# Optimization experiments

Measured on AMD Instinct MI355X. Metric: run time of the kernel, lower is better.

## Reference

```python
import jax, jax.numpy as jnp
import numpy as np

CDIM = 32
SCALES = (1, 16, 64, 256, 1024, 4096)  # last entry == T
INV_TEMP = 100.0
ENT_W = 0.1
COMMIT_W = 0.2
Q_SCALE = 1.0 / float(np.sqrt(CDIM))


def _interp_area(x, pt):
    # x: [B, T, C] -> [B, pt, C]; T divisible by pt so 'area' == block mean
    B, T, C = x.shape
    return x.reshape(B, pt, T // pt, C).mean(axis=2)


def _interp_linear(x, T):
    # x: [B, pt, C] -> [B, T, C]; mode='linear', align_corners=False
    pt = x.shape[1]
    pos = (jnp.arange(T, dtype=jnp.float32) + 0.5) * (pt / T) - 0.5
    pos = jnp.clip(pos, 0.0, pt - 1.0)
    lo = jnp.floor(pos).astype(jnp.int32)
    hi = jnp.minimum(lo + 1, pt - 1)
    w = (pos - lo.astype(jnp.float32))[None, :, None]
    return x[:, lo] * (1.0 - w) + x[:, hi] * w


def _bsq(f):
    # L2 normalize (torch F.normalize: clamp_min on norm)
    f = f / jnp.maximum(jnp.linalg.norm(f, axis=-1, keepdims=True), 1e-12)
    # sign quantize with STE
    zhat = jnp.where(f > 0, Q_SCALE, -Q_SCALE).astype(f.dtype)
    quantized = f + jax.lax.stop_gradient(zhat - f)
    # soft entropy loss
    p = jax.nn.sigmoid(-4.0 * f * (INV_TEMP / float(np.sqrt(CDIM))))
    prob = jnp.stack([p, 1.0 - p], axis=-1)  # [B, T, C, 2]
    ent = lambda c: -(c * jnp.log(c + 1e-8)).sum(axis=-1)
    per_sample_entropy = ent(prob).sum(axis=-1).mean()
    avg_prob = prob.mean(axis=(0, 1))  # [C, 2]
    cb_entropy = ent(avg_prob).sum()
    entropy_penalty = (per_sample_entropy - cb_entropy) / INV_TEMP
    commit = ((jax.lax.stop_gradient(quantized) - f) ** 2).sum(axis=-1).mean()
    aux = entropy_penalty * ENT_W + commit * COMMIT_W
    bits = (quantized > 0).astype(jnp.int32)
    return quantized, bits, aux


def setup_inputs() -> dict:
    key = jax.random.key(0)
    B, T, C = 128, SCALES[-1], CDIM
    return {"f_BTC": jax.random.normal(key, (B, T, C), dtype=jnp.float32)}


def reference(f_BTC):
    B, T, C = f_BTC.shape
    quantized_out = jnp.zeros_like(f_BTC)
    residual = f_BTC
    losses, bit_list = [], []
    for pt in SCALES:
        interp_res = _interp_area(residual, pt) if pt != T else residual
        q, bits, loss = _bsq(interp_res)
        q = _interp_linear(q, T) if pt != T else q
        residual = residual - jax.lax.stop_gradient(q)
        quantized_out = quantized_out + q
        bit_list.append(bits)
        losses.append(loss)
    all_losses = jnp.stack(losses, axis=-1)       # [num_scales]
    all_bits = jnp.concatenate(bit_list, axis=1)  # [B, sum(SCALES), C]
    return quantized_out, all_bits, all_losses
```

## Files before the change

### kernel.cpp

```cpp
#include <hip/hip_runtime.h>
#include <hip/hip_bf16.h>
#include <cstddef>
#include <cstdint>

#define NB 128
#define NT 4096
#define NC 32
#define BITROWS 5457
#define QV_ROWS 1361
#define QOUT_ELEMS (NB*NT*NC)
#define BITS_ELEMS (NB*BITROWS*NC)

#define ACC_OFF  22298624
#define S16_OFF  22302720

__device__ __constant__ float kQSC = 0.17677669529663687f;
__device__ __constant__ float kSIG = 17.67766952966369f;

__device__ __forceinline__ float interp_eval(const float* __restrict__ q, int P, int t, int c) {
  float pos = ((float)t + 0.5f) * ((float)P * (1.0f / 4096.0f)) - 0.5f;
  pos = fminf(fmaxf(pos, 0.0f), (float)(P - 1));
  const int lo = (int)pos;
  const int hi = min(lo + 1, P - 1);
  const float w = pos - (float)lo;
  const float a = __fmul_rn(q[lo * NC + c], 1.0f - w);
  const float b = __fmul_rn(q[hi * NC + c], w);
  return __fadd_rn(a, b);
}

__device__ __forceinline__ float interp_slice(const float* __restrict__ q, int P, int base, int t, int c) {
  float pos = ((float)t + 0.5f) * ((float)P * (1.0f / 4096.0f)) - 0.5f;
  pos = fminf(fmaxf(pos, 0.0f), (float)(P - 1));
  const int lo = (int)pos;
  const int hi = min(lo + 1, P - 1);
  const float w = pos - (float)lo;
  const float a = __fmul_rn(q[(lo - base) * NC + c], 1.0f - w);
  const float b = __fmul_rn(q[(hi - base) * NC + c], w);
  return __fadd_rn(a, b);
}

__device__ __forceinline__ void process_elem(
    float msum, float invn, int b, int rowOff, int j, int c,
    float* qlsRow, float* __restrict__ qvG, float* __restrict__ bitsG,
    float& entA, float& comA, float& pA)
{
  const float m = msum * invn;
  float ss = m * m;
  #pragma unroll
  for (int mk = 16; mk; mk >>= 1) ss += __shfl_xor(ss, mk, 32);
  const float den = fmaxf(sqrtf(ss), 1e-12f);
  const float fn = m / den;
  const bool bit = fn > 0.0f;
  const float zh = bit ? kQSC : -kQSC;
  const float qvv = fn + (zh - fn);
  if (qlsRow) qlsRow[c] = qvv;
  if (qvG) qvG[(size_t)b * (QV_ROWS * NC) + (size_t)(rowOff + j) * NC + c] = qvv;
  bitsG[(size_t)b * (BITROWS * NC) + (size_t)(rowOff + j) * NC + c] = bit ? 1.0f : 0.0f;
  const float arg = (-4.0f * fn) * kSIG;
  const float p = 1.0f / (1.0f + __expf(-arg));
  const float ent = -(p * __logf(p + 1e-8f) + (1.0f - p) * __logf((1.0f - p) + 1e-8f));
  const float d = qvv - fn;
  entA += ent; comA += d * d; pA += p;
}

__device__ __forceinline__ void reduce_losses(
    int sIdx, float entA, float comA, float pA, int tid, int nWaves,
    double* __restrict__ acc, float* redE, float* redC, float* redP)
{
  float e = entA, cm = comA;
  #pragma unroll
  for (int mk = 32; mk; mk >>= 1) { e += __shfl_xor(e, mk, 64); cm += __shfl_xor(cm, mk, 64); }
  const float p = pA + __shfl_xor(pA, 32, 64);
  const int w = tid >> 6, lane = tid & 63;
  if (lane == 0) { redE[w] = e; redC[w] = cm; }
  if (lane < 32) redP[w * 32 + lane] = p;
  __syncthreads();
  if (tid == 0) {
    double te = 0.0, tc = 0.0;
    for (int i = 0; i < nWaves; ++i) { te += (double)redE[i]; tc += (double)redC[i]; }
    atomicAdd(&acc[sIdx], te);
    atomicAdd(&acc[6 + sIdx], tc);
  }
  if (tid < 32) {
    float tp = 0.0f;
    for (int i = 0; i < nWaves; ++i) tp += redP[i * 32 + tid];
    atomicAdd(&acc[12 + sIdx * 32 + tid], (double)tp);
  }
  __syncthreads();
}

__global__ __launch_bounds__(256) void k_sum16(const float* __restrict__ f, float* __restrict__ S16) {
  const int idx = blockIdx.x * 256 + threadIdx.x;
  if (idx >= NB * 256 * NC) return;
  const int c = idx & 31;
  const int j = (idx >> 5) & 255;
  const int b = idx >> 13;
  const float* p = f + (size_t)b * (NT * NC) + (size_t)j * 16 * NC + c;
  float s = 0.0f;
  #pragma unroll
  for (int k = 0; k < 16; ++k) s += p[k * NC];
  S16[idx] = s;
}

__global__ __launch_bounds__(1024) void k_s0(
    const float* __restrict__ S16g, float* __restrict__ qv,
    float* __restrict__ bitsOut, double* __restrict__ acc)
{
  __shared__ float red[1024];
  __shared__ float redE[16], redC[16], redP[16 * 32];
  const int b = blockIdx.x, tid = threadIdx.x, c = tid & 31;
  const float* __restrict__ sb = S16g + (size_t)b * 8192;
  {
    const int g = tid >> 5;
    float part = 0.0f;
    #pragma unroll
    for (int j = 0; j < 8; ++j) part += sb[(size_t)(g * 8 + j) * NC + c];
    red[tid] = part;
  }
  __syncthreads();
  float entA = 0.0f, comA = 0.0f, pA = 0.0f;
  if (tid < 32) {
    float msum = 0.0f;
    for (int g = 0; g < 32; ++g) msum += red[g * 32 + tid];
    process_elem(msum, 1.0f / 4096.0f, b, 0, 0, tid, nullptr, qv, bitsOut, entA, comA, pA);
  }
  reduce_losses(0, entA, comA, pA, tid, 16, acc, redE, redC, redP);
}

__global__ __launch_bounds__(1024) void k_coarse2(
    const float* __restrict__ S16g,
    float* __restrict__ qv, float* __restrict__ bitsOut, double* __restrict__ acc)
{
  __shared__ float S[144 * NC];
  __shared__ float q1s[10 * NC];
  __shared__ float q2s[34 * NC];
  __shared__ float redE[16], redC[16], redP[16 * 32];
  const int b = blockIdx.x >> 1, seg = blockIdx.x & 1;
  const int tid = threadIdx.x, c = tid & 31;
  const int start = seg * 112;
  const int base1 = 8 * seg - 1, base2 = 32 * seg - 1;
  const float* __restrict__ sb = S16g + (size_t)b * 8192;
  const float* __restrict__ qb = qv + (size_t)b * (QV_ROWS * NC);

  for (int e = tid; e < 144 * NC; e += 1024)
    S[e] = sb[(size_t)(start + (e >> 5)) * NC + (e & 31)];
  __syncthreads();

  const float corr = 16.0f * qb[c];
  for (int e = tid; e < 144 * NC; e += 1024) S[e] -= corr;
  __syncthreads();

  float entA, comA, pA;

  entA = comA = pA = 0.0f;
  if (tid < 256) {
    const int jl = tid >> 5;
    const int j = 8 * seg + jl;
    float msum = 0.0f;
    for (int jj = 0; jj < 16; ++jj) msum += S[(j * 16 + jj - start) * NC + c];
    process_elem(msum, 1.0f / 256.0f, b, 1, j, c, &q1s[(j - base1) * NC], qv, bitsOut, entA, comA, pA);
  } else if (tid < 288) {
    const int jh = seg ? 7 : 8;
    float msum = 0.0f;
    for (int jj = 0; jj < 16; ++jj) msum += S[(jh * 16 + jj - start) * NC + c];
    const float m = msum * (1.0f / 256.0f);
    float ss = m * m;
    #pragma unroll
    for (int mk = 16; mk; mk >>= 1) ss += __shfl_xor(ss, mk, 32);
    const float den = fmaxf(sqrtf(ss), 1e-12f);
    const float fn = m / den;
    const float zh = (fn > 0.0f) ? kQSC : -kQSC;
    q1s[(jh - base1) * NC + c] = fn + (zh - fn);
  }
  reduce_losses(1, entA, comA, pA, tid, 16, acc, redE, redC, redP);

  {
    const int gc0 = seg ? 124 : 0;
    for (int e = tid; e < 132 * NC; e += 1024) {
      const int g = gc0 + (e >> 5);
      float cs = 0.0f;
      #pragma unroll
      for (int k = 0; k < 16; ++k) cs += interp_slice(q1s, 16, base1, g * 16 + k, c);
      S[(g - start) * NC + c] -= cs;
    }
  }
  __syncthreads();

  entA = comA = pA = 0.0f;
  {
    const int j2 = 32 * seg + (tid >> 5);
    float msum = 0.0f;
    #pragma unroll
    for (int jj = 0; jj < 4; ++jj) msum += S[(j2 * 4 + jj - start) * NC + c];
    process_elem(msum, 1.0f / 64.0f, b, 17, j2, c, &q2s[(j2 - base2) * NC], qv, bitsOut, entA, comA, pA);
  }
  if (tid < 32) {
    const int j2h = seg ? 31 : 32;
    float msum = 0.0f;
    #pragma unroll
    for (int jj = 0; jj < 4; ++jj) msum += S[(j2h * 4 + jj - start) * NC + c];
    const float m = msum * (1.0f / 64.0f);
    float ss = m * m;
    #pragma unroll
    for (int mk = 16; mk; mk >>= 1) ss += __shfl_xor(ss, mk, 32);
    const float den = fmaxf(sqrtf(ss), 1e-12f);
    const float fn = m / den;
    const float zh = (fn > 0.0f) ? kQSC : -kQSC;
    q2s[(j2h - base2) * NC + c] = fn + (zh - fn);
  }
  reduce_losses(2, entA, comA, pA, tid, 16, acc, redE, redC, redP);

  for (int e = tid; e < 128 * NC; e += 1024) {
    const int g = 128 * seg + (e >> 5);
    float cs = 0.0f;
    #pragma unroll
    for (int k = 0; k < 16; ++k) cs += interp_slice(q2s, 64, base2, g * 16 + k, c);
    S[(g - start) * NC + c] -= cs;
  }
  __syncthreads();

  entA = comA = pA = 0.0f;
  for (int out = tid; out < 128 * NC; out += 1024) {
    const int g = 128 * seg + (out >> 5);
    process_elem(S[(g - start) * NC + c], 1.0f / 16.0f, b, 81, g, c, nullptr, qv, bitsOut, entA, comA, pA);
  }
  reduce_losses(3, entA, comA, pA, tid, 16, acc, redE, redC, redP);
}

__global__ __launch_bounds__(256) void k_s45(
    const float* __restrict__ f, const float* __restrict__ qv,
    float* __restrict__ qout, float* __restrict__ bitsOut, double* __restrict__ acc)
{
  __shared__ float ql0[NC];
  __shared__ float ql1[3 * NC];
  __shared__ float ql2[6 * NC];
  __shared__ float ql3[18 * NC];
  __shared__ float ql4[66 * NC];
  __shared__ float redE[4], redC[4], redP[4 * 32];
  const int b = blockIdx.x >> 4, seg = blockIdx.x & 15;
  const int tid = threadIdx.x, c = tid & 31, rloc = tid >> 5;
  const float* __restrict__ qb = qv + (size_t)b * (QV_ROWS * NC);
  const float* __restrict__ fb = f + (size_t)b * (NT * NC);
  const int b1 = seg - 1, b2 = 4 * seg - 1, b3 = 16 * seg - 1, b4 = 64 * seg - 1;
  if (tid < NC) ql0[tid] = qb[tid];
  for (int e = tid; e < 3 * NC; e += 256) {
    const int r = min(max(b1 + (e >> 5), 0), 15);
    ql1[e] = qb[(1 + r) * NC + (e & 31)];
  }
  for (int e = tid; e < 6 * NC; e += 256) {
    const int r = min(max(b2 + (e >> 5), 0), 63);
    ql2[e] = qb[(17 + r) * NC + (e & 31)];
  }
  for (int e = tid; e < 18 * NC; e += 256) {
    const int r = min(max(b3 + (e >> 5), 0), 255);
    ql3[e] = qb[(81 + r) * NC + (e & 31)];
  }
  __syncthreads();

  float entA4 = 0.0f, comA4 = 0.0f, pA4 = 0.0f;
  float entB = 0.0f, comB = 0.0f, pB = 0.0f;

  auto do_A = [&](int p, float rc[4], float qc[4]) {
    const int i = seg * 64 + p * 8 + rloc;
    const float* fp = fb + (size_t)i * 4 * NC + c;
    float msum = 0.0f;
    #pragma unroll
    for (int k = 0; k < 4; ++k) {
      const int t = i * 4 + k;
      const float q0 = ql0[c];
      const float q1 = interp_slice(ql1, 16,  b1, t, c);
      const float q2 = interp_slice(ql2, 64,  b2, t, c);
      const float q3 = interp_slice(ql3, 256, b3, t, c);
      float r = fp[k * NC];
      r -= q0; r -= q1; r -= q2; r -= q3;
      float qs = q0; qs += q1; qs += q2; qs += q3;
      rc[k] = r; qc[k] = qs;
      msum += r;
    }
    process_elem(msum, 0.25f, b, 337, i, c,
                 &ql4[(size_t)(i - b4) * NC], nullptr, bitsOut, entA4, comA4, pA4);
  };

  auto do_halo = [&](int hr) {
    const float* fp = fb + (size_t)hr * 4 * NC + c;
    float msum = 0.0f;
    #pragma unroll
    for (int k = 0; k < 4; ++k) {
      const int t = hr * 4 + k;
      float r = fp[k * NC];
      r -= ql0[c];
      r -= interp_slice(ql1, 16,  b1, t, c);
      r -= interp_slice(ql2, 64,  b2, t, c);
      r -= interp_slice(ql3, 256, b3, t, c);
      msum += r;
    }
    const float m = msum * 0.25f;
    float ss = m * m;
    #pragma unroll
    for (int mk = 16; mk; mk >>= 1) ss += __shfl_xor(ss, mk, 32);
    const float den = fmaxf(sqrtf(ss), 1e-12f);
    const float fn = m / den;
    const float zh = (fn > 0.0f) ? kQSC : -kQSC;
    ql4[(size_t)(hr - b4) * NC + c] = fn + (zh - fn);
  };

  auto do_B = [&](int p, const float rc[4], const float qc[4]) {
    const int i = seg * 64 + p * 8 + rloc;
    #pragma unroll
    for (int k = 0; k < 4; ++k) {
      const int t = i * 4 + k;
      const float q4 = interp_slice(ql4, 1024, b4, t, c);
      float r = rc[k];
      r -= q4;
      float qs = qc[k];
      qs += q4;
      float ss = r * r;
      #pragma unroll
      for (int mk = 16; mk; mk >>= 1) ss += __shfl_xor(ss, mk, 32);
      const float den = fmaxf(sqrtf(ss), 1e-12f);
      const float fn = r / den;
      const bool bit = fn > 0.0f;
      const float zh = bit ? kQSC : -kQSC;
      const float qvv = fn + (zh - fn);
      qout[(size_t)b * (NT * NC) + (size_t)t * NC + c] = qs + qvv;
      bitsOut[(size_t)b * (BITROWS * NC) + (size_t)(1361 + t) * NC + c] = bit ? 1.0f : 0.0f;
      const float arg = (-4.0f * fn) * kSIG;
      const float p2 = 1.0f / (1.0f + __expf(-arg));
      entB += -(p2 * __logf(p2 + 1e-8f) + (1.0f - p2) * __logf((1.0f - p2) + 1e-8f));
      const float d = qvv - fn;
      comB += d * d;
      pB += p2;
    }
  };

  float rAp[4], qsAp[4];
  float rAc[4], qsAc[4];

  do_A(0, rAp, qsAp);
  if (rloc == 0 && seg > 0) do_halo(64 * seg - 1);

  for (int p = 1; p < 8; ++p) {
    do_A(p, rAc, qsAc);
    __syncthreads();
    do_B(p - 1, rAp, qsAp);
    #pragma unroll
    for (int k = 0; k < 4; ++k) { rAp[k] = rAc[k]; qsAp[k] = qsAc[k]; }
  }
  if (rloc == 1 && seg < 15) do_halo(64 * seg + 64);
  __syncthreads();
  do_B(7, rAp, qsAp);

  reduce_losses(4, entA4, comA4, pA4, tid, 4, acc, redE, redC, redP);
  reduce_losses(5, entB, comB, pB, tid, 4, acc, redE, redC, redP);
}

__global__ void k_losses(const double* __restrict__ acc, float* __restrict__ out) {
  const int s = threadIdx.x;
  if (s >= 6) return;
  const int pts[6] = {1, 16, 64, 256, 1024, 4096};
  const double n = 128.0 * (double)pts[s];
  const double pse = acc[s] / n;
  const double commit = acc[6 + s] / n;
  double cbe = 0.0;
  for (int c = 0; c < 32; ++c) {
    const double ap = acc[12 + s * 32 + c] / n;
    cbe += -(ap * log(ap + 1e-8) + (1.0 - ap) * log((1.0 - ap) + 1e-8));
  }
  const double pen = (pse - cbe) / 100.0;
  out[s] = (float)(pen * 0.1 + commit * 0.2);
}

extern "C" void kernel_launch(void* const* d_in, const int* in_sizes, int n_in,
                              void* d_out, int out_size, void* d_ws, size_t ws_size,
                              hipStream_t stream) {
  const float* f = (const float*)d_in[0];
  float* qout = (float*)d_out;
  float* bitsOut = qout + QOUT_ELEMS;
  float* lossesOut = qout + (QOUT_ELEMS + BITS_ELEMS);
  float* qv = (float*)d_ws;
  double* acc = (double*)((char*)d_ws + ACC_OFF);
  float* S16 = (float*)((char*)d_ws + S16_OFF);

  hipMemsetAsync(acc, 0, 204 * sizeof(double), stream);
  k_sum16<<<4096, 256, 0, stream>>>(f, S16);
  k_s0<<<NB, 1024, 0, stream>>>(S16, qv, bitsOut, acc);
  k_coarse2<<<NB * 2, 1024, 0, stream>>>(S16, qv, bitsOut, acc);
  k_s45<<<NB * 16, 256, 0, stream>>>(f, qv, qout, bitsOut, acc);
  k_losses<<<1, 64, 0, stream>>>(acc, lossesOut);
}
```

Baseline: 320.6 us.

## Fuse coarse scales into the fine-scale kernel with redundant halo recompute

The separate k_coarse2 kernel for scales 16/64/256 is removed. Each k_fused block now recomputes its own local slice of those coarse scales from S16, including halo rows, in shared memory before handling scales 1024/4096. This drops one launch, the coarse kernel's low-parallelism 256-block phase, and the global round-trip of the intermediate quantized values. The cost is redundant recomputation of halo rows across the 16 segments of each batch.

```diff
diff --git a/kernel.cpp b/kernel.cpp
--- a/kernel.cpp
+++ b/kernel.cpp
@@ -16,17 +16,6 @@
 
 __device__ __constant__ float kQSC = 0.17677669529663687f;
 __device__ __constant__ float kSIG = 17.67766952966369f;
-
-__device__ __forceinline__ float interp_eval(const float* __restrict__ q, int P, int t, int c) {
-  float pos = ((float)t + 0.5f) * ((float)P * (1.0f / 4096.0f)) - 0.5f;
-  pos = fminf(fmaxf(pos, 0.0f), (float)(P - 1));
-  const int lo = (int)pos;
-  const int hi = min(lo + 1, P - 1);
-  const float w = pos - (float)lo;
-  const float a = __fmul_rn(q[lo * NC + c], 1.0f - w);
-  const float b = __fmul_rn(q[hi * NC + c], w);
-  return __fadd_rn(a, b);
-}
 
 __device__ __forceinline__ float interp_slice(const float* __restrict__ q, int P, int base, int t, int c) {
   float pos = ((float)t + 0.5f) * ((float)P * (1.0f / 4096.0f)) - 0.5f;
@@ -63,6 +52,17 @@
   entA += ent; comA += d * d; pA += p;
 }
 
+__device__ __forceinline__ float quant_silent(float msum, float invn) {
+  const float m = msum * invn;
+  float ss = m * m;
+  #pragma unroll
+  for (int mk = 16; mk; mk >>= 1) ss += __shfl_xor(ss, mk, 32);
+  const float den = fmaxf(sqrtf(ss), 1e-12f);
+  const float fn = m / den;
+  const float zh = (fn > 0.0f) ? kQSC : -kQSC;
+  return fn + (zh - fn);
+}
+
 __device__ __forceinline__ void reduce_losses(
     int sIdx, float entA, float comA, float pA, int tid, int nWaves,
     double* __restrict__ acc, float* redE, float* redC, float* redP)
@@ -127,135 +127,95 @@
   reduce_losses(0, entA, comA, pA, tid, 16, acc, redE, redC, redP);
 }
 
-__global__ __launch_bounds__(1024) void k_coarse2(
-    const float* __restrict__ S16g,
-    float* __restrict__ qv, float* __restrict__ bitsOut, double* __restrict__ acc)
+__global__ __launch_bounds__(256) void k_fused(
+    const float* __restrict__ f, const float* __restrict__ S16g,
+    const float* __restrict__ qv, float* __restrict__ qout,
+    float* __restrict__ bitsOut, double* __restrict__ acc)
 {
-  __shared__ float S[144 * NC];
-  __shared__ float q1s[10 * NC];
-  __shared__ float q2s[34 * NC];
-  __shared__ float redE[16], redC[16], redP[16 * 32];
-  const int b = blockIdx.x >> 1, seg = blockIdx.x & 1;
-  const int tid = threadIdx.x, c = tid & 31;
-  const int start = seg * 112;
-  const int base1 = 8 * seg - 1, base2 = 32 * seg - 1;
-  const float* __restrict__ sb = S16g + (size_t)b * 8192;
-  const float* __restrict__ qb = qv + (size_t)b * (QV_ROWS * NC);
-
-  for (int e = tid; e < 144 * NC; e += 1024)
-    S[e] = sb[(size_t)(start + (e >> 5)) * NC + (e & 31)];
-  __syncthreads();
-
-  const float corr = 16.0f * qb[c];
-  for (int e = tid; e < 144 * NC; e += 1024) S[e] -= corr;
-  __syncthreads();
-
-  float entA, comA, pA;
-
-  entA = comA = pA = 0.0f;
-  if (tid < 256) {
-    const int jl = tid >> 5;
-    const int j = 8 * seg + jl;
-    float msum = 0.0f;
-    for (int jj = 0; jj < 16; ++jj) msum += S[(j * 16 + jj - start) * NC + c];
-    process_elem(msum, 1.0f / 256.0f, b, 1, j, c, &q1s[(j - base1) * NC], qv, bitsOut, entA, comA, pA);
-  } else if (tid < 288) {
-    const int jh = seg ? 7 : 8;
-    float msum = 0.0f;
-    for (int jj = 0; jj < 16; ++jj) msum += S[(jh * 16 + jj - start) * NC + c];
-    const float m = msum * (1.0f / 256.0f);
-    float ss = m * m;
-    #pragma unroll
-    for (int mk = 16; mk; mk >>= 1) ss += __shfl_xor(ss, mk, 32);
-    const float den = fmaxf(sqrtf(ss), 1e-12f);
-    const float fn = m / den;
-    const float zh = (fn > 0.0f) ? kQSC : -kQSC;
-    q1s[(jh - base1) * NC + c] = fn + (zh - fn);
-  }
-  reduce_losses(1, entA, comA, pA, tid, 16, acc, redE, redC, redP);
-
-  {
-    const int gc0 = seg ? 124 : 0;
-    for (int e = tid; e < 132 * NC; e += 1024) {
-      const int g = gc0 + (e >> 5);
-      float cs = 0.0f;
-      #pragma unroll
-      for (int k = 0; k < 16; ++k) cs += interp_slice(q1s, 16, base1, g * 16 + k, c);
-      S[(g - start) * NC + c] -= cs;
-    }
-  }
-  __syncthreads();
-
-  entA = comA = pA = 0.0f;
-  {
-    const int j2 = 32 * seg + (tid >> 5);
-    float msum = 0.0f;
-    #pragma unroll
-    for (int jj = 0; jj < 4; ++jj) msum += S[(j2 * 4 + jj - start) * NC + c];
-    process_elem(msum, 1.0f / 64.0f, b, 17, j2, c, &q2s[(j2 - base2) * NC], qv, bitsOut, entA, comA, pA);
-  }
-  if (tid < 32) {
-    const int j2h = seg ? 31 : 32;
-    float msum = 0.0f;
-    #pragma unroll
-    for (int jj = 0; jj < 4; ++jj) msum += S[(j2h * 4 + jj - start) * NC + c];
-    const float m = msum * (1.0f / 64.0f);
-    float ss = m * m;
-    #pragma unroll
-    for (int mk = 16; mk; mk >>= 1) ss += __shfl_xor(ss, mk, 32);
-    const float den = fmaxf(sqrtf(ss), 1e-12f);
-    const float fn = m / den;
-    const float zh = (fn > 0.0f) ? kQSC : -kQSC;
-    q2s[(j2h - base2) * NC + c] = fn + (zh - fn);
-  }
-  reduce_losses(2, entA, comA, pA, tid, 16, acc, redE, redC, redP);
-
-  for (int e = tid; e < 128 * NC; e += 1024) {
-    const int g = 128 * seg + (e >> 5);
-    float cs = 0.0f;
-    #pragma unroll
-    for (int k = 0; k < 16; ++k) cs += interp_slice(q2s, 64, base2, g * 16 + k, c);
-    S[(g - start) * NC + c] -= cs;
-  }
-  __syncthreads();
-
-  entA = comA = pA = 0.0f;
-  for (int out = tid; out < 128 * NC; out += 1024) {
-    const int g = 128 * seg + (out >> 5);
-    process_elem(S[(g - start) * NC + c], 1.0f / 16.0f, b, 81, g, c, nullptr, qv, bitsOut, entA, comA, pA);
-  }
-  reduce_losses(3, entA, comA, pA, tid, 16, acc, redE, redC, redP);
-}
-
-__global__ __launch_bounds__(256) void k_s45(
-    const float* __restrict__ f, const float* __restrict__ qv,
-    float* __restrict__ qout, float* __restrict__ bitsOut, double* __restrict__ acc)
-{
-  __shared__ float ql0[NC];
-  __shared__ float ql1[3 * NC];
-  __shared__ float ql2[6 * NC];
-  __shared__ float ql3[18 * NC];
+  __shared__ float S[48 * NC];
+  __shared__ float q1s[3 * NC];
+  __shared__ float q2s[6 * NC];
+  __shared__ float q3s[18 * NC];
   __shared__ float ql4[66 * NC];
   __shared__ float redE[4], redC[4], redP[4 * 32];
   const int b = blockIdx.x >> 4, seg = blockIdx.x & 15;
   const int tid = threadIdx.x, c = tid & 31, rloc = tid >> 5;
-  const float* __restrict__ qb = qv + (size_t)b * (QV_ROWS * NC);
   const float* __restrict__ fb = f + (size_t)b * (NT * NC);
+  const float* __restrict__ sb = S16g + (size_t)b * 8192;
   const int b1 = seg - 1, b2 = 4 * seg - 1, b3 = 16 * seg - 1, b4 = 64 * seg - 1;
-  if (tid < NC) ql0[tid] = qb[tid];
-  for (int e = tid; e < 3 * NC; e += 256) {
-    const int r = min(max(b1 + (e >> 5), 0), 15);
-    ql1[e] = qb[(1 + r) * NC + (e & 31)];
-  }
-  for (int e = tid; e < 6 * NC; e += 256) {
-    const int r = min(max(b2 + (e >> 5), 0), 63);
-    ql2[e] = qb[(17 + r) * NC + (e & 31)];
-  }
+  const int srow0 = 16 * seg - 16;
+  const float q0v = qv[(size_t)b * (QV_ROWS * NC) + c];
+
+  for (int e = tid; e < 48 * NC; e += 256) {
+    const int rw = min(max(srow0 + (e >> 5), 0), 255);
+    S[e] = sb[(size_t)rw * NC + (e & 31)] - 16.0f * q0v;
+  }
+  __syncthreads();
+
+  float ent = 0.0f, com = 0.0f, pp = 0.0f;
+
+  if (tid < 3 * NC) {
+    const int r = tid >> 5, j = b1 + r;
+    if (j >= 0 && j < 16) {
+      float msum = 0.0f;
+      for (int jj = 0; jj < 16; ++jj) msum += S[(j * 16 + jj - srow0) * NC + c];
+      if (r == 1)
+        process_elem(msum, 1.0f / 256.0f, b, 1, j, c, &q1s[r * NC], nullptr, bitsOut, ent, com, pp);
+      else
+        q1s[r * NC + c] = quant_silent(msum, 1.0f / 256.0f);
+    }
+  }
+  reduce_losses(1, ent, com, pp, tid, 4, acc, redE, redC, redP);
+
+  for (int e = tid; e < 24 * NC; e += 256) {
+    const int g = 16 * seg - 4 + (e >> 5);
+    if (g >= 0 && g < 256) {
+      float cs = 0.0f;
+      #pragma unroll
+      for (int k = 0; k < 16; ++k) cs += interp_slice(q1s, 16, b1, g * 16 + k, c);
+      S[(g - srow0) * NC + c] -= cs;
+    }
+  }
+  __syncthreads();
+
+  ent = com = pp = 0.0f;
+  if (tid < 6 * NC) {
+    const int r = tid >> 5, j2 = b2 + r;
+    if (j2 >= 0 && j2 < 64) {
+      float msum = 0.0f;
+      #pragma unroll
+      for (int jj = 0; jj < 4; ++jj) msum += S[(j2 * 4 + jj - srow0) * NC + c];
+      if (r >= 1 && r <= 4)
+        process_elem(msum, 1.0f / 64.0f, b, 17, j2, c, &q2s[r * NC], nullptr, bitsOut, ent, com, pp);
+      else
+        q2s[r * NC + c] = quant_silent(msum, 1.0f / 64.0f);
+    }
+  }
+  reduce_losses(2, ent, com, pp, tid, 4, acc, redE, redC, redP);
+
   for (int e = tid; e < 18 * NC; e += 256) {
-    const int r = min(max(b3 + (e >> 5), 0), 255);
-    ql3[e] = qb[(81 + r) * NC + (e & 31)];
-  }
-  __syncthreads();
+    const int g = 16 * seg - 1 + (e >> 5);
+    if (g >= 0 && g < 256) {
+      float cs = 0.0f;
+      #pragma unroll
+      for (int k = 0; k < 16; ++k) cs += interp_slice(q2s, 64, b2, g * 16 + k, c);
+      S[(g - srow0) * NC + c] -= cs;
+    }
+  }
+  __syncthreads();
+
+  ent = com = pp = 0.0f;
+  for (int e = tid; e < 18 * NC; e += 256) {
+    const int r = e >> 5, g = b3 + r;
+    if (g >= 0 && g < 256) {
+      const float ms = S[(g - srow0) * NC + c];
+      if (r >= 1 && r <= 16)
+        process_elem(ms, 1.0f / 16.0f, b, 81, g, c, &q3s[r * NC], nullptr, bitsOut, ent, com, pp);
+      else
+        q3s[r * NC + c] = quant_silent(ms, 1.0f / 16.0f);
+    }
+  }
+  reduce_losses(3, ent, com, pp, tid, 4, acc, redE, redC, redP);
 
   float entA4 = 0.0f, comA4 = 0.0f, pA4 = 0.0f;
   float entB = 0.0f, comB = 0.0f, pB = 0.0f;
@@ -267,10 +227,10 @@
     #pragma unroll
     for (int k = 0; k < 4; ++k) {
       const int t = i * 4 + k;
-      const float q0 = ql0[c];
-      const float q1 = interp_slice(ql1, 16,  b1, t, c);
-      const float q2 = interp_slice(ql2, 64,  b2, t, c);
-      const float q3 = interp_slice(ql3, 256, b3, t, c);
+      const float q0 = q0v;
+      const float q1 = interp_slice(q1s, 16,  b1, t, c);
+      const float q2 = interp_slice(q2s, 64,  b2, t, c);
+      const float q3 = interp_slice(q3s, 256, b3, t, c);
       float r = fp[k * NC];
       r -= q0; r -= q1; r -= q2; r -= q3;
       float qs = q0; qs += q1; qs += q2; qs += q3;
@@ -288,20 +248,13 @@
     for (int k = 0; k < 4; ++k) {
       const int t = hr * 4 + k;
       float r = fp[k * NC];
-      r -= ql0[c];
-      r -= interp_slice(ql1, 16,  b1, t, c);
-      r -= interp_slice(ql2, 64,  b2, t, c);
-      r -= interp_slice(ql3, 256, b3, t, c);
+      r -= q0v;
+      r -= interp_slice(q1s, 16,  b1, t, c);
+      r -= interp_slice(q2s, 64,  b2, t, c);
+      r -= interp_slice(q3s, 256, b3, t, c);
       msum += r;
     }
-    const float m = msum * 0.25f;
-    float ss = m * m;
-    #pragma unroll
-    for (int mk = 16; mk; mk >>= 1) ss += __shfl_xor(ss, mk, 32);
-    const float den = fmaxf(sqrtf(ss), 1e-12f);
-    const float fn = m / den;
-    const float zh = (fn > 0.0f) ? kQSC : -kQSC;
-    ql4[(size_t)(hr - b4) * NC + c] = fn + (zh - fn);
+    ql4[(size_t)(hr - b4) * NC + c] = quant_silent(msum, 0.25f);
   };
 
   auto do_B = [&](int p, const float rc[4], const float qc[4]) {
@@ -384,7 +337,6 @@
   hipMemsetAsync(acc, 0, 204 * sizeof(double), stream);
   k_sum16<<<4096, 256, 0, stream>>>(f, S16);
   k_s0<<<NB, 1024, 0, stream>>>(S16, qv, bitsOut, acc);
-  k_coarse2<<<NB * 2, 1024, 0, stream>>>(S16, qv, bitsOut, acc);
-  k_s45<<<NB * 16, 256, 0, stream>>>(f, qv, qout, bitsOut, acc);
+  k_fused<<<NB * 16, 256, 0, stream>>>(f, S16, qv, qout, bitsOut, acc);
   k_losses<<<1, 64, 0, stream>>>(acc, lossesOut);
 }
```

Result: slower. 390.5 us (+21.8%).
